# Optimization experiments

Measured on AMD Instinct MI355X. Metric: run time of the kernel, lower is better.

The kernel has to match this reference:

```python
import jax, jax.numpy as jnp
import numpy as np

D_MODEL = 1024
N_HEADS = 16
D_HEAD = D_MODEL // N_HEADS
EPS = 1e-6


def setup_inputs() -> dict:
    key = jax.random.key(0)
    ks = jax.random.split(key, 11)
    N, L, S = 4, 4096, 4096
    scale = 1.0 / np.sqrt(D_MODEL)
    inp = {
        "queries": jax.random.normal(ks[0], (N, L, D_MODEL), jnp.float32),
        "keys": jax.random.normal(ks[1], (N, S, D_MODEL), jnp.float32),
        "values": jax.random.normal(ks[2], (N, S, D_MODEL), jnp.float32),
        "Wq": jax.random.normal(ks[3], (D_MODEL, D_MODEL), jnp.float32) * scale,
        "bq": jnp.zeros((D_MODEL,), jnp.float32),
        "Wk": jax.random.normal(ks[4], (D_MODEL, D_MODEL), jnp.float32) * scale,
        "bk": jnp.zeros((D_MODEL,), jnp.float32),
        "Wv": jax.random.normal(ks[5], (D_MODEL, D_MODEL), jnp.float32) * scale,
        "bv": jnp.zeros((D_MODEL,), jnp.float32),
        "Wo": jax.random.normal(ks[6], (D_MODEL, D_MODEL), jnp.float32) * scale,
        "bo": jnp.zeros((D_MODEL,), jnp.float32),
    }
    return inp


def reference(queries, keys, values, Wq, bq, Wk, bk, Wv, bv, Wo, bo):
    N, L, _ = queries.shape
    S = keys.shape[1]
    H, Dh = N_HEADS, D_HEAD
    # projections (torch Linear: x @ W.T + b)
    q = (queries @ Wq.T + bq).reshape(N, L, H, Dh)
    k = (keys @ Wk.T + bk).reshape(N, S, H, Dh)
    v = (values @ Wv.T + bv).reshape(N, S, H, Dh)
    # elu+1 feature map
    Q = jax.nn.elu(q) + 1.0
    K = jax.nn.elu(k) + 1.0
    # KV summary: [N,H,Dv,Dh]
    KV = jnp.einsum('nshd,nshm->nhmd', K, v)
    # normalizer: [N,L,H]
    Z = 1.0 / (jnp.einsum('nlhd,nhd->nlh', Q, K.sum(axis=1)) + EPS)
    # output per head: [N,L,H,Dv]
    V = jnp.einsum('nlhd,nhmd,nlh->nlhm', Q, KV, Z)
    out = V.reshape(N, L, H * Dh) @ Wo.T + bo
    return out
```

## Files before the change

kernel.cpp:

```cpp
#include <hip/hip_runtime.h>
#include <hip/hip_bf16.h>

typedef __attribute__((ext_vector_type(8))) short short8;
typedef __attribute__((ext_vector_type(4))) short short4v;
typedef __attribute__((ext_vector_type(4))) float f32x4;

#define MFMA16(a, b, c) __builtin_amdgcn_mfma_f32_16x16x32_bf16(a, b, c, 0, 0, 0)

__device__ __forceinline__ unsigned short f2bf(float f) {
    unsigned int u = __float_as_uint(f);
    unsigned int r = u + 0x7fffu + ((u >> 16) & 1u);
    return (unsigned short)(r >> 16);
}
__device__ __forceinline__ float bf2f(unsigned short h) {
    return __uint_as_float(((unsigned int)h) << 16);
}

__device__ __forceinline__ void async16(const void* g, void* l) {
    __builtin_amdgcn_global_load_lds(
        (const __attribute__((address_space(1))) unsigned int*)g,
        (__attribute__((address_space(3))) unsigned int*)l, 16, 0, 0);
}

#define S_BARRIER() asm volatile("s_barrier" ::: "memory")
#define SCHED_FENCE() __builtin_amdgcn_sched_barrier(0)

__global__ __launch_bounds__(256) void cvt_all(const float* __restrict__ q,
                                               const float* __restrict__ k,
                                               const float* __restrict__ v,
                                               const float* __restrict__ Wq,
                                               const float* __restrict__ Wk,
                                               const float* __restrict__ Wv,
                                               const float* __restrict__ Wo,
                                               unsigned short* __restrict__ qb,
                                               unsigned short* __restrict__ kb,
                                               unsigned short* __restrict__ vb,
                                               unsigned short* __restrict__ Wqb,
                                               unsigned short* __restrict__ Wkb,
                                               unsigned short* __restrict__ Wvb,
                                               unsigned short* __restrict__ Wob) {
    int b = blockIdx.x;
    const float* in;
    unsigned short* out;
    int lb, nb, n4;
    if (b < 6144) {
        int s = b >> 11;
        lb = b & 2047; nb = 2048; n4 = 4194304;
        in = s == 0 ? q : s == 1 ? k : v;
        out = s == 0 ? qb : s == 1 ? kb : vb;
    } else {
        int s = b - 6144;
        int w = s >> 7;
        lb = s & 127; nb = 128; n4 = 262144;
        in = w == 0 ? Wq : w == 1 ? Wk : w == 2 ? Wv : Wo;
        out = w == 0 ? Wqb : w == 1 ? Wkb : w == 2 ? Wvb : Wob;
    }
    for (int i = lb * 256 + threadIdx.x; i < n4; i += nb * 256) {
        float4 vv = reinterpret_cast<const float4*>(in)[i];
        short4v p;
        p[0] = (short)f2bf(vv.x); p[1] = (short)f2bf(vv.y);
        p[2] = (short)f2bf(vv.z); p[3] = (short)f2bf(vv.w);
        reinterpret_cast<short4v*>(out)[i] = p;
    }
}

__device__ __forceinline__ void gemm_body(const unsigned short* __restrict__ A,
                                          const unsigned short* __restrict__ B,
                                          const float* __restrict__ bias,
                                          void* __restrict__ out,
                                          int mode, char* lds, int bid) {
    const int tid = threadIdx.x;
    const int lane = tid & 63, wid = tid >> 6;
    const int wr = wid >> 2, wc = wid & 3;
    const int lr = lane & 15, lg = lane >> 4;

    const int swz = (bid & 7) * 32 + (bid >> 3);
    const int bm = swz >> 2, bn = swz & 3;
    const long row0 = (long)bm * 256;
    const long col0 = (long)bn * 256;

    const unsigned short* srcA[2];
    const unsigned short* srcB[2];
    int dstOff[2];
#pragma unroll
    for (int g = 0; g < 2; ++g) {
        int s = g * 512 + tid;
        int pr = s >> 3;
        int dc = (s & 7) ^ (pr & 7);
        srcA[g] = A + (row0 + (pr & 63) + 128 * (pr >> 6)) * 1024 + dc * 8;
        srcB[g] = B + (col0 + pr) * 1024 + dc * 8;
        dstOff[g] = s * 16;
    }

#define STG_AQ(BB, Q, KT) do {                                                  \
        async16(srcA[0] + (Q) * 65536 + (KT) * 64,                              \
                lds + (BB) * 65536 + (Q) * 16384 + dstOff[0]);                  \
        async16(srcA[1] + (Q) * 65536 + (KT) * 64,                              \
                lds + (BB) * 65536 + (Q) * 16384 + dstOff[1]); } while (0)
#define STG_BH(BB, H, KT) do {                                                  \
        async16(srcB[0] + (H) * 131072 + (KT) * 64,                             \
                lds + (BB) * 65536 + 32768 + (H) * 16384 + dstOff[0]);          \
        async16(srcB[1] + (H) * 131072 + (KT) * 64,                             \
                lds + (BB) * 65536 + 32768 + (H) * 16384 + dstOff[1]); } while (0)

    const int ch0 = (((0 * 4 + lg) ^ (lr & 7)) << 4);
    const int ch1 = (((1 * 4 + lg) ^ (lr & 7)) << 4);
    const int aB0 = (64 * wr + lr) * 128 + ch0;
    const int aB1 = (64 * wr + lr) * 128 + ch1;
    const int bB0 = 32768 + (wc >> 1) * 16384 + ((wc & 1) * 64 + lr) * 128 + ch0;
    const int bB1 = 32768 + (wc >> 1) * 16384 + ((wc & 1) * 64 + lr) * 128 + ch1;

    f32x4 acc[8][4] = {};
    short8 b0[4], b1[4];

#define GATE4() do { asm volatile("s_waitcnt vmcnt(4)" ::: "memory"); SCHED_FENCE(); } while (0)
#define GATE0() do { asm volatile("s_waitcnt vmcnt(0)" ::: "memory"); SCHED_FENCE(); } while (0)
#define MFMA_BLOCK(MB, BV) do {                                                 \
        S_BARRIER();                                                            \
        asm volatile("s_waitcnt lgkmcnt(0)" ::: "memory");                      \
        SCHED_FENCE();                                                          \
        __builtin_amdgcn_s_setprio(1);                                          \
        _Pragma("unroll") for (int m = 0; m < 4; ++m)                           \
            _Pragma("unroll") for (int n = 0; n < 4; ++n)                       \
                acc[(MB) + m][n] = MFMA16(a[m], BV[n], acc[(MB) + m][n]);       \
        __builtin_amdgcn_s_setprio(0);                                          \
        SCHED_FENCE();                                                          \
        S_BARRIER(); } while (0)
#define LOAD_A(BUFB, ABASE, Q) do {                                             \
        _Pragma("unroll") for (int m = 0; m < 4; ++m)                           \
            a[m] = *(const short8*)(lds + (BUFB) + (Q) * 16384 + (ABASE) + m * 2048); } while (0)
#define LOAD_B(BUFB, BBASE, BV) do {                                            \
        _Pragma("unroll") for (int n = 0; n < 4; ++n)                           \
            BV[n] = *(const short8*)(lds + (BUFB) + (BBASE) + n * 2048); } while (0)

    STG_AQ(0, 0, 0); STG_BH(0, 0, 0); STG_BH(0, 1, 0); STG_AQ(0, 1, 0);
    STG_AQ(1, 0, 1); STG_BH(1, 0, 1);
    GATE4();
    S_BARRIER();

#pragma unroll 1
    for (int t = 0; t < 7; ++t) {
        const int ktA = 2 * t + 1, ktB = 2 * t + 2, ktC = 2 * t + 3;
        { short8 a[4]; LOAD_B(0, bB0, b0); LOAD_A(0, aB0, 0); STG_BH(1, 1, ktA); MFMA_BLOCK(0, b0); }
        { short8 a[4]; LOAD_B(0, bB1, b1); LOAD_A(0, aB1, 0); STG_AQ(1, 1, ktA); MFMA_BLOCK(0, b1); }
        { short8 a[4]; LOAD_A(0, aB0, 1); STG_AQ(0, 0, ktB); MFMA_BLOCK(4, b0); }
        { short8 a[4]; LOAD_A(0, aB1, 1); STG_BH(0, 0, ktB); GATE4(); MFMA_BLOCK(4, b1); }
        { short8 a[4]; LOAD_B(65536, bB0, b0); LOAD_A(65536, aB0, 0); STG_BH(0, 1, ktB); MFMA_BLOCK(0, b0); }
        { short8 a[4]; LOAD_B(65536, bB1, b1); LOAD_A(65536, aB1, 0); STG_AQ(0, 1, ktB); MFMA_BLOCK(0, b1); }
        { short8 a[4]; LOAD_A(65536, aB0, 1); STG_AQ(1, 0, ktC); MFMA_BLOCK(4, b0); }
        { short8 a[4]; LOAD_A(65536, aB1, 1); STG_BH(1, 0, ktC); GATE4(); MFMA_BLOCK(4, b1); }
    }
    {
        { short8 a[4]; LOAD_B(0, bB0, b0); LOAD_A(0, aB0, 0); STG_BH(1, 1, 15); MFMA_BLOCK(0, b0); }
        { short8 a[4]; LOAD_B(0, bB1, b1); LOAD_A(0, aB1, 0); STG_AQ(1, 1, 15); MFMA_BLOCK(0, b1); }
        { short8 a[4]; LOAD_A(0, aB0, 1); MFMA_BLOCK(4, b0); }
        { short8 a[4]; LOAD_A(0, aB1, 1); GATE0(); MFMA_BLOCK(4, b1); }
        { short8 a[4]; LOAD_B(65536, bB0, b0); LOAD_A(65536, aB0, 0); MFMA_BLOCK(0, b0); }
        { short8 a[4]; LOAD_B(65536, bB1, b1); LOAD_A(65536, aB1, 0); MFMA_BLOCK(0, b1); }
        { short8 a[4]; LOAD_A(65536, aB0, 1); MFMA_BLOCK(4, b0); }
        { short8 a[4]; LOAD_A(65536, aB1, 1); MFMA_BLOCK(4, b1); }
    }
#undef STG_AQ
#undef STG_BH
#undef GATE4
#undef GATE0
#undef MFMA_BLOCK
#undef LOAD_A
#undef LOAD_B

    const int r4 = lg * 4;
#pragma unroll
    for (int m = 0; m < 8; ++m) {
#pragma unroll
        for (int n = 0; n < 4; ++n) {
            long col = col0 + wc * 64 + n * 16 + lr;
            float bcol = bias[col];
            long R0 = row0 + wr * 128 + m * 16 + r4;
            if (mode == 0) {
                unsigned short* O = (unsigned short*)out;
#pragma unroll
                for (int j = 0; j < 4; ++j) {
                    float v = acc[m][n][j] + bcol;
                    v = v > 0.f ? v + 1.f : __expf(v);
                    O[(R0 + j) * 1024 + col] = f2bf(v);
                }
            } else if (mode == 1 || mode == 2) {
                unsigned short* O = (unsigned short*)out;
                long nb = R0 >> 12;
                long s = R0 & 4095;
                short4v pack;
#pragma unroll
                for (int j = 0; j < 4; ++j) {
                    float v = acc[m][n][j] + bcol;
                    if (mode == 1) v = v > 0.f ? v + 1.f : __expf(v);
                    pack[j] = (short)f2bf(v);
                }
                *(short4v*)(O + ((nb << 10) + col) * 4096 + s) = pack;
            } else {
                float* O = (float*)out;
#pragma unroll
                for (int j = 0; j < 4; ++j)
                    O[(R0 + j) * 1024 + col] = acc[m][n][j] + bcol;
            }
        }
    }
}

__global__ __launch_bounds__(512, 1) void proj_gemm(const unsigned short* __restrict__ qb,
                                                    const unsigned short* __restrict__ kb,
                                                    const unsigned short* __restrict__ vb,
                                                    const unsigned short* __restrict__ Wqb,
                                                    const unsigned short* __restrict__ Wkb,
                                                    const unsigned short* __restrict__ Wvb,
                                                    const float* __restrict__ bq,
                                                    const float* __restrict__ bk,
                                                    const float* __restrict__ bv,
                                                    unsigned short* __restrict__ Qm,
                                                    unsigned short* __restrict__ Kt,
                                                    unsigned short* __restrict__ vT) {
    __shared__ __align__(16) char lds[131072];
    int seg = blockIdx.x >> 8;
    int bid = blockIdx.x & 255;
    const unsigned short* A = seg == 0 ? qb : seg == 1 ? kb : vb;
    const unsigned short* B = seg == 0 ? Wqb : seg == 1 ? Wkb : Wvb;
    const float* bias = seg == 0 ? bq : seg == 1 ? bk : bv;
    void* out = seg == 0 ? (void*)Qm : seg == 1 ? (void*)Kt : (void*)vT;
    gemm_body(A, B, bias, out, seg, lds, bid);
}

__global__ __launch_bounds__(512, 1) void out_gemm(const unsigned short* __restrict__ Vbuf,
                                                   const unsigned short* __restrict__ Wob,
                                                   const float* __restrict__ bo,
                                                   float* __restrict__ out) {
    __shared__ __align__(16) char lds[131072];
    gemm_body(Vbuf, Wob, bo, out, 3, lds, blockIdx.x);
}

__global__ __launch_bounds__(256) void kv_kernel(const unsigned short* __restrict__ Kt,
                                                 const unsigned short* __restrict__ vT,
                                                 float* __restrict__ KV,
                                                 float* __restrict__ Ksum) {
    int b = blockIdx.x;
    int sc = b & 7, h = (b >> 3) & 15, n = b >> 7;
    const int tid = threadIdx.x, lane = tid & 63, wave = tid >> 6;
    long base = ((long)(n * 1024 + h * 64)) * 4096 + sc * 512;
    const unsigned short* Kp = Kt + base;
    const unsigned short* Vp = vT + base;
    const int lr = lane & 15, lk = (lane >> 4) * 8;

    f32x4 acc[4] = {};
    for (int s0 = 0; s0 < 512; s0 += 32) {
        short8 a = *(const short8*)(Vp + (long)(wave * 16 + lr) * 4096 + s0 + lk);
#pragma unroll
        for (int d4 = 0; d4 < 4; ++d4) {
            short8 bb = *(const short8*)(Kp + (long)(d4 * 16 + lr) * 4096 + s0 + lk);
            acc[d4] = MFMA16(a, bb, acc[d4]);
        }
    }
    float* KVb = KV + (long)(n * 16 + h) * 4096;
#pragma unroll
    for (int d4 = 0; d4 < 4; ++d4)
#pragma unroll
        for (int j = 0; j < 4; ++j) {
            int m = wave * 16 + (lane >> 4) * 4 + j;
            int d = d4 * 16 + lr;
            atomicAdd(KVb + m * 64 + d, acc[d4][j]);
        }
    int d = tid & 63, part = tid >> 6;
    const unsigned short* kp2 = Kt + ((long)(n * 1024 + h * 64 + d)) * 4096 + sc * 512 + part * 128;
    float s = 0.f;
    for (int i = 0; i < 128; i += 8) {
        short8 v = *(const short8*)(kp2 + i);
#pragma unroll
        for (int e = 0; e < 8; ++e) s += bf2f((unsigned short)v[e]);
    }
    atomicAdd(Ksum + n * 1024 + h * 64 + d, s);
}

__global__ __launch_bounds__(256) void attn_kernel(const unsigned short* __restrict__ Qm,
                                                   const float* __restrict__ KV,
                                                   const float* __restrict__ Ksum,
                                                   unsigned short* __restrict__ Vbuf) {
    __shared__ unsigned short Qs[128 * 64];
    __shared__ unsigned short KVs[64 * 64];
    __shared__ float zin[128];
    __shared__ float ks[64];
    int b = blockIdx.x;
    int lc = b & 31, h = (b >> 5) & 15, n = b >> 9;
    int tid = threadIdx.x, lane = tid & 63, wave = tid >> 6;
    long l0 = (long)n * 4096 + lc * 128;

    const unsigned short* Qg = Qm + (l0 + (tid >> 3)) * 1024 + h * 64 + (tid & 7) * 8;
    char* QsB = (char*)Qs + (wave << 10);
#pragma unroll
    for (int it = 0; it < 4; ++it)
        async16(Qg + (long)it * 32 * 1024, QsB + it * 4096);

    const float* kvp = KV + (long)(n * 16 + h) * 4096;
    for (int i = tid * 4; i < 4096; i += 1024) {
        float4 v = *reinterpret_cast<const float4*>(kvp + i);
        short4v p;
        p[0] = (short)f2bf(v.x); p[1] = (short)f2bf(v.y);
        p[2] = (short)f2bf(v.z); p[3] = (short)f2bf(v.w);
        *(short4v*)(KVs + i) = p;
    }
    if (tid < 64) ks[tid] = Ksum[n * 1024 + h * 64 + tid];
    __syncthreads();

    {
        int row = tid >> 1, half = tid & 1;
        float den = 0.f;
        const unsigned short* qrow = Qs + row * 64 + half * 32;
#pragma unroll
        for (int d = 0; d < 32; ++d) den += bf2f(qrow[d]) * ks[half * 32 + d];
        den += __shfl_xor(den, 1, 64);
        if (half == 0) zin[row] = 1.0f / (den + 1e-6f);
    }
    __syncthreads();

    const int lr = lane & 15, lk = (lane >> 4) * 8;
    f32x4 acc[2][4] = {};
#pragma unroll
    for (int kk = 0; kk < 2; ++kk) {
        short8 a0 = *(const short8*)(Qs + (wave * 32 + lr) * 64 + kk * 32 + lk);
        short8 a1 = *(const short8*)(Qs + (wave * 32 + 16 + lr) * 64 + kk * 32 + lk);
#pragma unroll
        for (int nn = 0; nn < 4; ++nn) {
            short8 bb = *(const short8*)(KVs + (nn * 16 + lr) * 64 + kk * 32 + lk);
            acc[0][nn] = MFMA16(a0, bb, acc[0][nn]);
            acc[1][nn] = MFMA16(a1, bb, acc[1][nn]);
        }
    }
#pragma unroll
    for (int mi = 0; mi < 2; ++mi)
#pragma unroll
        for (int nn = 0; nn < 4; ++nn)
#pragma unroll
            for (int j = 0; j < 4; ++j) {
                int rl = wave * 32 + mi * 16 + (lane >> 4) * 4 + j;
                int mcol = nn * 16 + lr;
                float v = acc[mi][nn][j] * zin[rl];
                Vbuf[(l0 + rl) * 1024 + h * 64 + mcol] = f2bf(v);
            }
}

extern "C" void kernel_launch(void* const* d_in, const int* in_sizes, int n_in,
                              void* d_out, int out_size, void* d_ws, size_t ws_size,
                              hipStream_t stream) {
    const float* queries = (const float*)d_in[0];
    const float* keys    = (const float*)d_in[1];
    const float* values  = (const float*)d_in[2];
    const float* Wq = (const float*)d_in[3];
    const float* bq = (const float*)d_in[4];
    const float* Wk = (const float*)d_in[5];
    const float* bk = (const float*)d_in[6];
    const float* Wv = (const float*)d_in[7];
    const float* bv = (const float*)d_in[8];
    const float* Wo = (const float*)d_in[9];
    const float* bo = (const float*)d_in[10];
    float* out = (float*)d_out;

    char* ws = (char*)d_ws;
    const size_t SZ = (size_t)16384 * 1024 * 2;
    const size_t WSZ = (size_t)1024 * 1024 * 2;
    unsigned short* qb  = (unsigned short*)(ws);
    unsigned short* kb  = (unsigned short*)(ws + SZ);
    unsigned short* vb  = (unsigned short*)(ws + 2 * SZ);
    unsigned short* Wqb = (unsigned short*)(ws + 3 * SZ);
    unsigned short* Wkb = (unsigned short*)(ws + 3 * SZ + WSZ);
    unsigned short* Wvb = (unsigned short*)(ws + 3 * SZ + 2 * WSZ);
    unsigned short* Wob = (unsigned short*)(ws + 3 * SZ + 3 * WSZ);
    unsigned short* Qm  = (unsigned short*)(ws + 3 * SZ + 4 * WSZ);
    unsigned short* Kt  = (unsigned short*)(ws + 4 * SZ + 4 * WSZ);
    unsigned short* vT  = (unsigned short*)(ws + 5 * SZ + 4 * WSZ);
    float* KVf = (float*)(ws + 6 * SZ + 4 * WSZ);
    float* Ksf = (float*)(ws + 6 * SZ + 4 * WSZ + 1048576);
    unsigned short* Vbuf = qb;

    cvt_all<<<6656, 256, 0, stream>>>(queries, keys, values, Wq, Wk, Wv, Wo,
                                      qb, kb, vb, Wqb, Wkb, Wvb, Wob);

    proj_gemm<<<768, 512, 0, stream>>>(qb, kb, vb, Wqb, Wkb, Wvb, bq, bk, bv, Qm, Kt, vT);

    hipMemsetAsync(KVf, 0, 1048576 + 16384, stream);
    kv_kernel<<<512, 256, 0, stream>>>(Kt, vT, KVf, Ksf);
    attn_kernel<<<2048, 256, 0, stream>>>(Qm, KVf, Ksf, Vbuf);

    out_gemm<<<256, 512, 0, stream>>>(Vbuf, Wob, bo, out);
}
```

Measured before the change: 257.0 us.

## Stage GEMM and attention epilogues through LDS for vectorized stores; fuse Ksum into KV

The mode 0 and mode 3 GEMM epilogues and the attention-kernel epilogue now write accumulators to a per-wave LDS scratch tile. They read the tile back row-contiguous and emit 16-byte global stores, replacing the scattered 2- or 4-byte stores. The fp32-to-bf16 convert kernel now processes 8 elements per thread with 16-byte stores. The K column sum is folded into the KV MFMA loop using the B fragments already in registers, which removes a second pass over Kt. The costs are extra LDS traffic, waitcnt fences in the epilogue, and reuse of LDS regions that the main loops previously occupied.

```diff
diff --git a/kernel.cpp b/kernel.cpp
--- a/kernel.cpp
+++ b/kernel.cpp
@@ -14,6 +14,9 @@
 }
 __device__ __forceinline__ float bf2f(unsigned short h) {
     return __uint_as_float(((unsigned int)h) << 16);
+}
+__device__ __forceinline__ unsigned int pk2(float lo, float hi) {
+    return (unsigned int)f2bf(lo) | ((unsigned int)f2bf(hi) << 16);
 }
 
 __device__ __forceinline__ void async16(const void* g, void* l) {
@@ -42,25 +45,26 @@
     int b = blockIdx.x;
     const float* in;
     unsigned short* out;
-    int lb, nb, n4;
+    int lb, nb, n8;
     if (b < 6144) {
         int s = b >> 11;
-        lb = b & 2047; nb = 2048; n4 = 4194304;
+        lb = b & 2047; nb = 2048; n8 = 2097152;
         in = s == 0 ? q : s == 1 ? k : v;
         out = s == 0 ? qb : s == 1 ? kb : vb;
     } else {
         int s = b - 6144;
         int w = s >> 7;
-        lb = s & 127; nb = 128; n4 = 262144;
+        lb = s & 127; nb = 128; n8 = 131072;
         in = w == 0 ? Wq : w == 1 ? Wk : w == 2 ? Wv : Wo;
         out = w == 0 ? Wqb : w == 1 ? Wkb : w == 2 ? Wvb : Wob;
     }
-    for (int i = lb * 256 + threadIdx.x; i < n4; i += nb * 256) {
-        float4 vv = reinterpret_cast<const float4*>(in)[i];
-        short4v p;
-        p[0] = (short)f2bf(vv.x); p[1] = (short)f2bf(vv.y);
-        p[2] = (short)f2bf(vv.z); p[3] = (short)f2bf(vv.w);
-        reinterpret_cast<short4v*>(out)[i] = p;
+    for (int i = lb * 256 + threadIdx.x; i < n8; i += nb * 256) {
+        float4 v0 = reinterpret_cast<const float4*>(in)[2 * i];
+        float4 v1 = reinterpret_cast<const float4*>(in)[2 * i + 1];
+        uint4 p;
+        p.x = pk2(v0.x, v0.y); p.y = pk2(v0.z, v0.w);
+        p.z = pk2(v1.x, v1.y); p.w = pk2(v1.z, v1.w);
+        reinterpret_cast<uint4*>(out)[i] = p;
     }
 }
 
@@ -169,22 +173,55 @@
 #undef LOAD_B
 
     const int r4 = lg * 4;
-#pragma unroll
-    for (int m = 0; m < 8; ++m) {
-#pragma unroll
-        for (int n = 0; n < 4; ++n) {
-            long col = col0 + wc * 64 + n * 16 + lr;
-            float bcol = bias[col];
-            long R0 = row0 + wr * 128 + m * 16 + r4;
+    if (mode == 0 || mode == 3) {
+        char* ep = lds + wid * 4608;
+#pragma unroll
+        for (int m = 0; m < 8; ++m) {
+#pragma unroll
+            for (int n = 0; n < 4; ++n) {
+                float bcol = bias[col0 + wc * 64 + n * 16 + lr];
+#pragma unroll
+                for (int j = 0; j < 4; ++j) {
+                    float v = acc[m][n][j] + bcol;
+                    if (mode == 0) v = v > 0.f ? v + 1.f : __expf(v);
+                    *(float*)(ep + (((lg * 4 + j) * 68) + n * 16 + lr) * 4) = v;
+                }
+            }
+            asm volatile("s_waitcnt lgkmcnt(0)" ::: "memory");
+            SCHED_FENCE();
+            long R0b = row0 + wr * 128 + m * 16;
             if (mode == 0) {
                 unsigned short* O = (unsigned short*)out;
 #pragma unroll
-                for (int j = 0; j < 4; ++j) {
-                    float v = acc[m][n][j] + bcol;
-                    v = v > 0.f ? v + 1.f : __expf(v);
-                    O[(R0 + j) * 1024 + col] = f2bf(v);
+                for (int i = 0; i < 2; ++i) {
+                    int r = i * 8 + (lane >> 3), c8 = (lane & 7) * 8;
+                    float4 u0 = *(const float4*)(ep + (r * 68 + c8) * 4);
+                    float4 u1 = *(const float4*)(ep + (r * 68 + c8 + 4) * 4);
+                    uint4 w;
+                    w.x = pk2(u0.x, u0.y); w.y = pk2(u0.z, u0.w);
+                    w.z = pk2(u1.x, u1.y); w.w = pk2(u1.z, u1.w);
+                    *(uint4*)(O + (R0b + r) * 1024 + col0 + wc * 64 + c8) = w;
                 }
-            } else if (mode == 1 || mode == 2) {
+            } else {
+                float* O = (float*)out;
+#pragma unroll
+                for (int i = 0; i < 4; ++i) {
+                    int r = i * 4 + (lane >> 4), c4 = (lane & 15) * 4;
+                    float4 u = *(const float4*)(ep + (r * 68 + c4) * 4);
+                    *(float4*)(O + (R0b + r) * 1024 + col0 + wc * 64 + c4) = u;
+                }
+            }
+            asm volatile("s_waitcnt lgkmcnt(0)" ::: "memory");
+            SCHED_FENCE();
+        }
+    } else {
+#pragma unroll
+        for (int m = 0; m < 8; ++m) {
+#pragma unroll
+            for (int n = 0; n < 4; ++n) {
+                long col = col0 + wc * 64 + n * 16 + lr;
+                float bcol = bias[col];
+                long R0 = row0 + wr * 128 + m * 16 + r4;
                 unsigned short* O = (unsigned short*)out;
                 long nb = R0 >> 12;
                 long s = R0 & 4095;
@@ -196,11 +233,6 @@
                     pack[j] = (short)f2bf(v);
                 }
                 *(short4v*)(O + ((nb << 10) + col) * 4096 + s) = pack;
-            } else {
-                float* O = (float*)out;
-#pragma unroll
-                for (int j = 0; j < 4; ++j)
-                    O[(R0 + j) * 1024 + col] = acc[m][n][j] + bcol;
             }
         }
     }
@@ -249,12 +281,19 @@
     const int lr = lane & 15, lk = (lane >> 4) * 8;
 
     f32x4 acc[4] = {};
+    float ksa[4] = {0.f, 0.f, 0.f, 0.f};
     for (int s0 = 0; s0 < 512; s0 += 32) {
         short8 a = *(const short8*)(Vp + (long)(wave * 16 + lr) * 4096 + s0 + lk);
 #pragma unroll
         for (int d4 = 0; d4 < 4; ++d4) {
             short8 bb = *(const short8*)(Kp + (long)(d4 * 16 + lr) * 4096 + s0 + lk);
             acc[d4] = MFMA16(a, bb, acc[d4]);
+            if (wave == 0) {
+                float t = 0.f;
+#pragma unroll
+                for (int e = 0; e < 8; ++e) t += bf2f((unsigned short)bb[e]);
+                ksa[d4] += t;
+            }
         }
     }
     float* KVb = KV + (long)(n * 16 + h) * 4096;
@@ -266,15 +305,15 @@
             int d = d4 * 16 + lr;
             atomicAdd(KVb + m * 64 + d, acc[d4][j]);
         }
-    int d = tid & 63, part = tid >> 6;
-    const unsigned short* kp2 = Kt + ((long)(n * 1024 + h * 64 + d)) * 4096 + sc * 512 + part * 128;
-    float s = 0.f;
-    for (int i = 0; i < 128; i += 8) {
-        short8 v = *(const short8*)(kp2 + i);
-#pragma unroll
-        for (int e = 0; e < 8; ++e) s += bf2f((unsigned short)v[e]);
-    }
-    atomicAdd(Ksum + n * 1024 + h * 64 + d, s);
+    if (wave == 0) {
+#pragma unroll
+        for (int d4 = 0; d4 < 4; ++d4) {
+            float t = ksa[d4];
+            t += __shfl_xor(t, 16, 64);
+            t += __shfl_xor(t, 32, 64);
+            if (lane < 16) atomicAdd(Ksum + n * 1024 + h * 64 + d4 * 16 + lane, t);
+        }
+    }
 }
 
 __global__ __launch_bounds__(256) void attn_kernel(const unsigned short* __restrict__ Qm,
@@ -331,17 +370,35 @@
             acc[1][nn] = MFMA16(a1, bb, acc[1][nn]);
         }
     }
-#pragma unroll
-    for (int mi = 0; mi < 2; ++mi)
-#pragma unroll
-        for (int nn = 0; nn < 4; ++nn)
-#pragma unroll
-            for (int j = 0; j < 4; ++j) {
-                int rl = wave * 32 + mi * 16 + (lane >> 4) * 4 + j;
-                int mcol = nn * 16 + lr;
-                float v = acc[mi][nn][j] * zin[rl];
-                Vbuf[(l0 + rl) * 1024 + h * 64 + mcol] = f2bf(v);
+
+    {
+        char* ep = (char*)Qs + wave * 4096;
+#pragma unroll
+        for (int mi = 0; mi < 2; ++mi) {
+#pragma unroll
+            for (int nn = 0; nn < 4; ++nn)
+#pragma unroll
+                for (int j = 0; j < 4; ++j) {
+                    int rloc = (lane >> 4) * 4 + j;
+                    float v = acc[mi][nn][j] * zin[wave * 32 + mi * 16 + rloc];
+                    *(float*)(ep + (rloc * 64 + nn * 16 + lr) * 4) = v;
+                }
+            asm volatile("s_waitcnt lgkmcnt(0)" ::: "memory");
+            SCHED_FENCE();
+#pragma unroll
+            for (int i = 0; i < 2; ++i) {
+                int r = i * 8 + (lane >> 3), c8 = (lane & 7) * 8;
+                float4 u0 = *(const float4*)(ep + (r * 64 + c8) * 4);
+                float4 u1 = *(const float4*)(ep + (r * 64 + c8 + 4) * 4);
+                uint4 w;
+                w.x = pk2(u0.x, u0.y); w.y = pk2(u0.z, u0.w);
+                w.z = pk2(u1.x, u1.y); w.w = pk2(u1.z, u1.w);
+                *(uint4*)(Vbuf + (l0 + wave * 32 + mi * 16 + r) * 1024 + h * 64 + c8) = w;
             }
+            asm volatile("s_waitcnt lgkmcnt(0)" ::: "memory");
+            SCHED_FENCE();
+        }
+    }
 }
 
 extern "C" void kernel_launch(void* const* d_in, const int* in_sizes, int n_in,
```

After: 251.5 us. -2.1%, faster.
